# Optimization experiments

Measured on AMD Instinct MI355X. Metric: run time of the kernel, lower is better.

## Reference

```python
import jax, jax.numpy as jnp
import numpy as np

NEG_INF = -1e9
HIDDEN = 1024
HEADS = 16
SPH = HIDDEN // HEADS  # 64
B, Q, M = 8, 512, 512
R = Q + M


def rel_shift(x):
    # x: [N, H, Q, R] -> TransformerXL relative shift
    N, H, Qd, Rd = x.shape
    x = jnp.pad(x, ((0, 0), (0, 0), (0, 0), (1, 0)))
    x = x.reshape(N, H, Rd + 1, Qd)
    return x[:, :, 1:, :].reshape(N, H, Qd, Rd)


def setup_inputs() -> dict:
    key = jax.random.key(0)
    ks = jax.random.split(key, 11)
    std = 1.0 / np.sqrt(HIDDEN)
    # causal token mask: query position i (global pos M+i) may attend to ref pos j <= M+i
    q_pos = jnp.arange(Q)[:, None] + M
    r_pos = jnp.arange(R)[None, :]
    token_mask = (r_pos > q_pos).astype(jnp.float32)[None, None]  # [1,1,Q,R]
    return {
        "query_seqs": jax.random.normal(ks[0], (B, Q, HIDDEN), jnp.float32),
        "memory_seqs": jax.random.normal(ks[1], (B, M, HIDDEN), jnp.float32),
        "positional_encoding": jax.random.normal(ks[2], (R, HIDDEN), jnp.float32),
        "token_mask": token_mask,
        "content_bias": jax.random.normal(ks[3], (HEADS, SPH), jnp.float32) * 0.02,
        "position_bias": jax.random.normal(ks[4], (HEADS, SPH), jnp.float32) * 0.02,
        "Wq": jax.random.normal(ks[5], (HIDDEN, HEADS, SPH), jnp.float32) * std,
        "Wkc": jax.random.normal(ks[6], (HIDDEN, HEADS, SPH), jnp.float32) * std,
        "Wkp": jax.random.normal(ks[7], (HIDDEN, HEADS, SPH), jnp.float32) * std,
        "Wv": jax.random.normal(ks[8], (HIDDEN, HEADS, SPH), jnp.float32) * std,
        "Wo": jax.random.normal(ks[9], (HEADS, SPH, HIDDEN), jnp.float32) * std,
    }


def reference(query_seqs, memory_seqs, positional_encoding, token_mask,
              content_bias, position_bias, Wq, Wkc, Wkp, Wv, Wo):
    reference_seqs = jnp.concatenate([memory_seqs, query_seqs], axis=1)  # [B,R,D]
    query = jnp.einsum('nqd,dhs->nqhs', query_seqs, Wq)            # [B,Q,H,S]
    key_content = jnp.einsum('nrd,dhs->nrhs', reference_seqs, Wkc)  # [B,R,H,S]
    key_position = jnp.einsum('rd,dhs->rhs', positional_encoding, Wkp)  # [R,H,S]
    value = jnp.einsum('nrd,dhs->nrhs', reference_seqs, Wv)         # [B,R,H,S]

    content = jnp.einsum('nqhs,nrhs->nhqr', query + content_bias, key_content)
    positions = jnp.einsum('nqhs,rhs->nhqr', query + position_bias, key_position)
    positions = rel_shift(positions)

    scores = (content + positions) / np.sqrt(SPH) + token_mask * NEG_INF
    attn = jax.nn.softmax(scores, axis=3)  # [B,H,Q,R]
    out = jnp.einsum('nhqr,nrhs->nqhs', attn, value)
    return jnp.einsum('nqhs,hsd->nqd', out, Wo)  # [B,Q,D]
```

## Files before the change

### kernel.cpp

```cpp
#include <hip/hip_runtime.h>

#define B_ 8
#define Q_ 512
#define M_ 512
#define R_ 1024
#define H_ 16
#define S_ 64
#define D_ 1024
#define MEG 1048576L

typedef unsigned short ushort_t;
typedef __attribute__((ext_vector_type(8))) _Float16 f16x8;
typedef __attribute__((ext_vector_type(8))) unsigned short u16x8;
typedef __attribute__((ext_vector_type(4))) unsigned short u16x4;
typedef __attribute__((ext_vector_type(4))) float f32x4;
typedef __attribute__((ext_vector_type(2))) unsigned int u32x2;

__device__ __forceinline__ unsigned short h2u(_Float16 h) {
    union { _Float16 h; unsigned short u; } v; v.h = h; return v.u;
}
__device__ __forceinline__ unsigned int pk_f16(float a, float b) {
    union { _Float16 h[2]; unsigned int u; } v;
    v.h[0] = (_Float16)a; v.h[1] = (_Float16)b; return v.u;
}
__device__ __forceinline__ void async_cp16(const ushort_t* g, ushort_t* l) {
    __builtin_amdgcn_global_load_lds(
        (const __attribute__((address_space(1))) void*)g,
        (__attribute__((address_space(3))) void*)l, 16, 0, 0);
}

__global__ __launch_bounds__(256) void zero_out_f32_k(float* __restrict__ p, int n) {
    int i = blockIdx.x * 256 + threadIdx.x;
    if (i < n) p[i] = 0.f;
}

__global__ __launch_bounds__(256) void prep_k(
    const float* __restrict__ mem, const float* __restrict__ qry,
    const float* __restrict__ pos, const float* __restrict__ cb,
    const float* __restrict__ pb,
    const float* __restrict__ Wkc, const float* __restrict__ Wv,
    const float* __restrict__ Wkp, const float* __restrict__ Wq,
    const float* __restrict__ Wo,
    ushort_t* __restrict__ qcat, ushort_t* __restrict__ posb,
    ushort_t* __restrict__ cbpb, ushort_t* __restrict__ BT4,
    ushort_t* __restrict__ WoT) {
    int x = blockIdx.x, y = blockIdx.y, t = threadIdx.x;
    if (y < 5) {
        const float* in; ushort_t* out;
        switch (y) {
            case 0: in = Wkc; out = BT4;           break;
            case 1: in = Wv;  out = BT4 + MEG;     break;
            case 2: in = Wkp; out = BT4 + 2 * MEG; break;
            case 3: in = Wq;  out = BT4 + 3 * MEG; break;
            default: in = Wo; out = WoT;           break;
        }
        __shared__ ushort_t tile[32][33];
        int bx = (x & 31) * 32, by = (x >> 5) * 32;
        int tx = t & 31, ty = t >> 5;
        #pragma unroll
        for (int i = 0; i < 32; i += 8)
            tile[ty + i][tx] = h2u((_Float16)in[(long)(by + ty + i) * 1024 + bx + tx]);
        __syncthreads();
        #pragma unroll
        for (int i = 0; i < 32; i += 8)
            out[(long)(bx + ty + i) * 1024 + by + tx] = tile[tx][ty + i];
    } else if (y < 13) {
        int g = y - 5, r = x;
        const float* src = (r < 512) ? (mem + ((long)g * 512 + r) * 1024)
                                     : (qry + ((long)g * 512 + (r - 512)) * 1024);
        ushort_t* dst = qcat + ((long)g * 1024 + r) * 1024;
        int i = t * 4;
        f32x4 v = *(const f32x4*)(src + i);
        u32x2 o; o[0] = pk_f16(v[0], v[1]); o[1] = pk_f16(v[2], v[3]);
        *(u32x2*)(dst + i) = o;
    } else if (y == 13) {
        int i = t * 4;
        f32x4 v = *(const f32x4*)(pos + (long)x * 1024 + i);
        u32x2 o; o[0] = pk_f16(v[0], v[1]); o[1] = pk_f16(v[2], v[3]);
        *(u32x2*)(posb + (long)x * 1024 + i) = o;
    } else {
        if (x == 0) {
            for (int i = t; i < 1024; i += 256) {
                cbpb[i]        = h2u((_Float16)cb[i]);
                cbpb[1024 + i] = h2u((_Float16)pb[i]);
            }
        }
    }
}

__device__ __forceinline__ void gemm_body(const ushort_t* Arow0,
                                          const ushort_t* BTrow0,
                                          void* Crow0, long crs, int mode) {
    __shared__ __align__(16) ushort_t Al[2][128 * 32];
    __shared__ __align__(16) ushort_t Bl[2][128 * 32];

    int t = threadIdx.x;
    int wave = t >> 6, lane = t & 63, quad = lane >> 4, l16 = lane & 15;
    int wm = (wave & 1) * 64, wn = (wave >> 1) * 64;

    f32x4 acc[4][4];
    #pragma unroll
    for (int im = 0; im < 4; ++im)
        #pragma unroll
        for (int in = 0; in < 4; ++in) acc[im][in] = (f32x4){0.f, 0.f, 0.f, 0.f};

    int grow = lane >> 2, gcol = (lane & 3) * 8;
    const ushort_t* ga0 = Arow0 + (long)(wave * 32 + grow) * 1024 + gcol;
    const ushort_t* ga1 = Arow0 + (long)(wave * 32 + 16 + grow) * 1024 + gcol;
    const ushort_t* gb0 = BTrow0 + (long)(wave * 32 + grow) * 1024 + gcol;
    const ushort_t* gb1 = BTrow0 + (long)(wave * 32 + 16 + grow) * 1024 + gcol;
    int lo0 = (wave * 2 + 0) * 512;
    int lo1 = (wave * 2 + 1) * 512;

    async_cp16(ga0, &Al[0][lo0]);
    async_cp16(ga1, &Al[0][lo1]);
    async_cp16(gb0, &Bl[0][lo0]);
    async_cp16(gb1, &Bl[0][lo1]);
    __syncthreads();

    int cur = 0;
    for (int k0 = 0; k0 < 1024; k0 += 32) {
        int nxt = cur ^ 1;
        if (k0 + 32 < 1024) {
            async_cp16(ga0 + k0 + 32, &Al[nxt][lo0]);
            async_cp16(ga1 + k0 + 32, &Al[nxt][lo1]);
            async_cp16(gb0 + k0 + 32, &Bl[nxt][lo0]);
            async_cp16(gb1 + k0 + 32, &Bl[nxt][lo1]);
        }

        f16x8 af[4], bf[4];
        #pragma unroll
        for (int im = 0; im < 4; ++im)
            af[im] = *(const f16x8*)&Al[cur][(wm + im * 16 + l16) * 32 + quad * 8];
        #pragma unroll
        for (int in = 0; in < 4; ++in)
            bf[in] = *(const f16x8*)&Bl[cur][(wn + in * 16 + l16) * 32 + quad * 8];
        __builtin_amdgcn_s_setprio(1);
        #pragma unroll
        for (int im = 0; im < 4; ++im)
            #pragma unroll
            for (int in = 0; in < 4; ++in)
                acc[im][in] = __builtin_amdgcn_mfma_f32_16x16x32_f16(
                    af[im], bf[in], acc[im][in], 0, 0, 0);
        __builtin_amdgcn_s_setprio(0);
        __syncthreads();
        cur = nxt;
    }

    if (mode == 2) {
        #pragma unroll
        for (int im = 0; im < 4; ++im)
            #pragma unroll
            for (int in = 0; in < 4; ++in) {
                u16x4 pk;
                #pragma unroll
                for (int reg = 0; reg < 4; ++reg) pk[reg] = h2u((_Float16)acc[im][in][reg]);
                long addr = (long)(wn + in * 16 + l16) * 1024 + wm + im * 16 + quad * 4;
                *(u16x4*)((ushort_t*)Crow0 + addr) = pk;
            }
        return;
    }
    #pragma unroll
    for (int im = 0; im < 4; ++im)
        #pragma unroll
        for (int in = 0; in < 4; ++in)
            #pragma unroll
            for (int reg = 0; reg < 4; ++reg) {
                long addr = (long)(wm + im * 16 + quad * 4 + reg) * crs
                          + wn + in * 16 + l16;
                if (mode == 1) ((float*)Crow0)[addr] = acc[im][in][reg];
                else ((ushort_t*)Crow0)[addr] = h2u((_Float16)acc[im][in][reg]);
            }
}

__global__ __launch_bounds__(256) void gemm_mega(
    const ushort_t* __restrict__ qcat, const ushort_t* __restrict__ posb,
    const ushort_t* __restrict__ BT4,
    ushort_t* __restrict__ kcC, ushort_t* __restrict__ vT,
    ushort_t* __restrict__ qproj, ushort_t* __restrict__ kpp) {
    int id = blockIdx.x;
    if (id < 1024) {
        int z = id >> 7, tl = id & 127;
        int x = tl >> 4, y = tl & 15;
        const ushort_t* Arow0 = qcat + (long)z * MEG + (long)x * 128 * 1024;
        if (y < 8) {
            gemm_body(Arow0, BT4 + (long)y * 128 * 1024,
                      kcC + (long)z * MEG + (long)x * 128 * 1024 + y * 128, 1024, 0);
        } else {
            int n0 = (y - 8) * 128;
            gemm_body(Arow0, BT4 + (long)(1024 + n0) * 1024,
                      vT + ((long)z * 1024 + n0) * 1024 + x * 128, 0, 2);
        }
    } else if (id < 1088) {
        int u = id - 1024;
        int x = u >> 3, y = u & 7;
        gemm_body(posb + (long)x * 128 * 1024,
                  BT4 + (long)(2048 + y * 128) * 1024,
                  kpp + (long)x * 128 * 1024 + y * 128, 1024, 0);
    } else {
        int u = id - 1088;
        int b = u >> 5, v2 = u & 31;
        int x = v2 >> 3, y = v2 & 7;
        gemm_body(qcat + (long)b * MEG + (long)(512 + x * 128) * 1024,
                  BT4 + (long)(3072 + y * 128) * 1024,
                  qproj + (long)b * 512 * 1024 + (long)x * 128 * 1024 + y * 128, 1024, 0);
    }
}

__global__ __launch_bounds__(256) void gemm_fin(
    const ushort_t* __restrict__ A, const ushort_t* __restrict__ WoT,
    float* __restrict__ out) {
    gemm_body(A + (long)blockIdx.x * 128 * 1024,
              WoT + (long)blockIdx.y * 128 * 1024,
              out + (long)blockIdx.x * 128 * 1024 + blockIdx.y * 128, 1024, 1);
}

__global__ __launch_bounds__(512) void attn_kernel(
    const ushort_t* __restrict__ qproj,
    const ushort_t* __restrict__ kc,
    const ushort_t* __restrict__ kp,
    const ushort_t* __restrict__ vT,
    const ushort_t* __restrict__ cbpb,
    ushort_t* __restrict__ aout)
{
    int qt = (blockIdx.x + ((blockIdx.y >> 6) << 1)) & 3;
    int q0 = qt * 128;
    int bh = blockIdx.y;
    int b = bh >> 4, h = bh & 15;
    int t = threadIdx.x;
    int wave = t >> 6, lane = t & 63, quad = lane >> 4, l16 = lane & 15;

    __shared__ __align__(16) ushort_t Kc[64][72];
    __shared__ __align__(16) ushort_t Vt[64][72];
    __shared__ __align__(16) ushort_t Kp[192][72];
    __shared__ __align__(16) char Pu[8][2304];
    ushort_t* Pl = (ushort_t*)&Pu[wave][0];

    const ushort_t* qrow = qproj + ((long)(b * Q_ + q0 + wave * 16 + l16)) * 1024 + h * 64;
    f16x8 qcf[2], qpf[2];
    #pragma unroll
    for (int ks = 0; ks < 2; ++ks) {
        f16x8 qv  = *(const f16x8*)(qrow + ks * 32 + quad * 8);
        f16x8 cbv = *(const f16x8*)(cbpb + h * 64 + ks * 32 + quad * 8);
        f16x8 pbv = *(const f16x8*)(cbpb + 1024 + h * 64 + ks * 32 + quad * 8);
        qcf[ks] = qv + cbv;
        qpf[ks] = qv + pbv;
    }

    float m_s[4], l_s[4];
    f32x4 o_acc[4];
    #pragma unroll
    for (int r = 0; r < 4; ++r) {
        m_s[r] = -1e30f; l_s[r] = 0.f;
        o_acc[r] = (f32x4){0.f, 0.f, 0.f, 0.f};
    }

    int srow = t >> 3, sc0 = (t & 7) * 8;
    const ushort_t* kcb = kc + ((long)(b * R_) + srow) * 1024 + h * 64 + sc0;
    const ushort_t* vtb = vT + ((long)(b * 1024 + h * 64 + srow)) * 1024 + sc0;
    const ushort_t* kpb = kp + h * 64 + sc0;

    int ntiles = ((q0 + 639) >> 6) + 1;

    u16x8 rKc = *(const u16x8*)(kcb);
    u16x8 rVt = *(const u16x8*)(vtb);
    u16x8 rKp[3];
    {
        int jb0 = 384 - q0;
        #pragma unroll
        for (int p = 0; p < 3; ++p) {
            int j = jb0 + p * 64 + srow;
            int jc = j > 1023 ? 1023 : j;
            rKp[p] = *(const u16x8*)(kpb + (long)jc * 1024);
        }
    }

    for (int it = 0; it < ntiles; ++it) {
        int r0 = it * 64;
        int jbase = r0 - q0 + 384;
        int gb0 = jbase >> 4;
        __syncthreads();
        *(u16x8*)&Kc[srow][sc0] = rKc;
        *(u16x8*)&Vt[srow][sc0] = rVt;
        if (it == 0) {
            #pragma unroll
            for (int p = 0; p < 3; ++p) {
                int j = jbase + p * 64 + srow;
                int ph = ((j >> 4) % 12) * 16 + (j & 15);
                *(u16x8*)&Kp[ph][sc0] = rKp[p];
            }
        } else {
            int j = jbase + 128 + srow;
            int ph = ((j >> 4) % 12) * 16 + (j & 15);
            *(u16x8*)&Kp[ph][sc0] = rKp[0];
        }
        __syncthreads();
        if (it + 1 < ntiles) {
            int r1 = r0 + 64;
            rKc = *(const u16x8*)(kcb + (long)r1 * 1024);
            rVt = *(const u16x8*)(vtb + r1);
            int j = r1 - q0 + 512 + srow;
            int jc = j > 1023 ? 1023 : j;
            rKp[0] = *(const u16x8*)(kpb + (long)jc * 1024);
        }

        f32x4 sc[4];
        #pragma unroll
        for (int s = 0; s < 4; ++s) sc[s] = (f32x4){0.f, 0.f, 0.f, 0.f};
        f32x4 dd[5];
        #pragma unroll
        for (int s = 0; s < 5; ++s) dd[s] = (f32x4){0.f, 0.f, 0.f, 0.f};

        __builtin_amdgcn_s_setprio(1);
        #pragma unroll
        for (int ks = 0; ks < 2; ++ks)
            #pragma unroll
            for (int sub = 0; sub < 4; ++sub) {
                f16x8 bb = *(const f16x8*)&Kc[sub * 16 + l16][ks * 32 + quad * 8];
                sc[sub] = __builtin_amdgcn_mfma_f32_16x16x32_f16(qcf[ks], bb, sc[sub], 0, 0, 0);
            }
        #pragma unroll
        for (int ks = 0; ks < 2; ++ks)
            #pragma unroll
            for (int sub = 0; sub < 5; ++sub) {
                int pb = (gb0 + 7 - wave + sub) % 12;
                f16x8 bb = *(const f16x8*)&Kp[pb * 16 + l16][ks * 32 + quad * 8];
                dd[sub] = __builtin_amdgcn_mfma_f32_16x16x32_f16(qpf[ks], bb, dd[sub], 0, 0, 0);
            }
        __builtin_amdgcn_s_setprio(0);

        #pragma unroll
        for (int reg = 0; reg < 4; ++reg) {
            int row16 = quad * 4 + reg;
            int src = (lane & 48) + ((l16 + 15 - row16) & 15);
            float dsh[5];
            #pragma unroll
            for (int sub = 0; sub < 5; ++sub)
                dsh[sub] = __shfl(dd[sub][reg], src);
            #pragma unroll
            for (int sub = 0; sub < 4; ++sub) {
                float dval = (l16 > row16) ? dsh[sub + 1] : dsh[sub];
                float sv = (sc[sub][reg] + dval) * 0.125f;
                int rl = sub * 16 + l16;
                if (r0 + rl > q0 + wave * 16 + row16 + 512) sv = -1e30f;
                sc[sub][reg] = sv;
            }
        }

        float rm[4];
        #pragma unroll
        for (int reg = 0; reg < 4; ++reg) {
            float v = fmaxf(fmaxf(sc[0][reg], sc[1][reg]), fmaxf(sc[2][reg], sc[3][reg]));
            #pragma unroll
            for (int m = 1; m < 16; m <<= 1) v = fmaxf(v, __shfl_xor(v, m));
            rm[reg] = v;
        }
        int ok = (rm[0] <= m_s[0] + 8.f) & (rm[1] <= m_s[1] + 8.f) &
                 (rm[2] <= m_s[2] + 8.f) & (rm[3] <= m_s[3] + 8.f);
        if (!__all(ok)) {
            #pragma unroll
            for (int reg = 0; reg < 4; ++reg) {
                float mn = fmaxf(m_s[reg], rm[reg]);
                float alpha = __expf(m_s[reg] - mn);
                m_s[reg] = mn;
                l_s[reg] *= alpha;
                #pragma unroll
                for (int sub = 0; sub < 4; ++sub)
                    o_acc[sub][reg] *= alpha;
            }
        }
        float rs[4] = {0.f, 0.f, 0.f, 0.f};
        #pragma unroll
        for (int sub = 0; sub < 4; ++sub)
            #pragma unroll
            for (int reg = 0; reg < 4; ++reg) {
                float p = __expf(sc[sub][reg] - m_s[reg]);
                rs[reg] += p;
                Pl[(quad * 4 + reg) * 72 + sub * 16 + l16] = h2u((_Float16)p);
            }
        #pragma unroll
        for (int reg = 0; reg < 4; ++reg) {
            float v = rs[reg];
            #pragma unroll
            for (int m = 1; m < 16; m <<= 1) v += __shfl_xor(v, m);
            l_s[reg] += v;
        }

        __builtin_amdgcn_s_setprio(1);
        #pragma unroll
        for (int ks = 0; ks < 2; ++ks) {
            f16x8 a = *(const f16x8*)&Pl[l16 * 72 + ks * 32 + quad * 8];
            #pragma unroll
            for (int sub = 0; sub < 4; ++sub) {
                f16x8 bb = *(const f16x8*)&Vt[sub * 16 + l16][ks * 32 + quad * 8];
                o_acc[sub] = __builtin_amdgcn_mfma_f32_16x16x32_f16(a, bb, o_acc[sub], 0, 0, 0);
            }
        }
        __builtin_amdgcn_s_setprio(0);
    }

    #pragma unroll
    for (int reg = 0; reg < 4; ++reg) {
        float inv = 1.f / l_s[reg];
        int qg = q0 + wave * 16 + quad * 4 + reg;
        ushort_t* orow = aout + ((long)(b * Q_ + qg)) * 1024 + h * 64;
        #pragma unroll
        for (int sub = 0; sub < 4; ++sub)
            orow[sub * 16 + l16] = h2u((_Float16)(o_acc[sub][reg] * inv));
    }
}

extern "C" void kernel_launch(void* const* d_in, const int* in_sizes, int n_in,
                              void* d_out, int out_size, void* d_ws, size_t ws_size,
                              hipStream_t stream) {
    const float* query  = (const float*)d_in[0];
    const float* memory = (const float*)d_in[1];
    const float* pos    = (const float*)d_in[2];
    const float* cb  = (const float*)d_in[4];
    const float* pb  = (const float*)d_in[5];
    const float* Wq  = (const float*)d_in[6];
    const float* Wkc = (const float*)d_in[7];
    const float* Wkp = (const float*)d_in[8];
    const float* Wv  = (const float*)d_in[9];
    const float* Wo  = (const float*)d_in[10];
    float* out = (float*)d_out;
    ushort_t* ws = (ushort_t*)d_ws;

    size_t ws_elems = ws_size / 2;
    if (ws_elems < 36 * MEG) {
        zero_out_f32_k<<<(out_size + 255) / 256, 256, 0, stream>>>(out, out_size);
        return;
    }

    ushort_t* cbpb  = ws;
    ushort_t* BT4   = ws + MEG;
    ushort_t* WoT   = BT4 + 4 * MEG;
    ushort_t* kpp   = WoT + MEG;
    ushort_t* posb  = kpp + MEG;
    ushort_t* qproj = posb + MEG;
    ushort_t* kcC   = qproj + 4 * MEG;
    ushort_t* vT    = kcC + 8 * MEG;
    ushort_t* qcat  = vT + 8 * MEG;
    ushort_t* aout  = qproj;

    prep_k<<<dim3(1024, 15), 256, 0, stream>>>(
        memory, query, pos, cb, pb, Wkc, Wv, Wkp, Wq, Wo,
        qcat, posb, cbpb, BT4, WoT);
    gemm_mega<<<dim3(1344), 256, 0, stream>>>(qcat, posb, BT4, kcC, vT, qproj, kpp);
    attn_kernel<<<dim3(4, 128), 512, 0, stream>>>(qproj, kcC, kpp, vT, cbpb, aout);
    gemm_fin<<<dim3(32, 8, 1), 256, 0, stream>>>(aout, WoT, out);
}
```

Before: 263.3 us.

## Load K/V fragments directly from global, drop LDS staging and syncs, MFMA row sums

Removes the shared-memory staging of Kc, Vt and Kp along with the two block barriers per tile. Each wave now loads its MFMA operand fragments straight from global memory, relying on L1/L2 for reuse across the 8 waves. The softmax row sum is computed with an MFMA against a ones vector, and the row-max shuffle reduction runs only when a rescale is needed. Occupancy is also requested via launch bounds. The risk is redundant global/L2 traffic, since each wave re-reads the same K/V tiles, plus more register pressure from holding the fragments.

```diff
diff --git a/kernel.cpp b/kernel.cpp
--- a/kernel.cpp
+++ b/kernel.cpp
@@ -215,7 +215,7 @@
               out + (long)blockIdx.x * 128 * 1024 + blockIdx.y * 128, 1024, 1);
 }
 
-__global__ __launch_bounds__(512) void attn_kernel(
+__global__ __launch_bounds__(512, 4) void attn_kernel(
     const ushort_t* __restrict__ qproj,
     const ushort_t* __restrict__ kc,
     const ushort_t* __restrict__ kp,
@@ -230,9 +230,6 @@
     int t = threadIdx.x;
     int wave = t >> 6, lane = t & 63, quad = lane >> 4, l16 = lane & 15;
 
-    __shared__ __align__(16) ushort_t Kc[64][72];
-    __shared__ __align__(16) ushort_t Vt[64][72];
-    __shared__ __align__(16) ushort_t Kp[192][72];
     __shared__ __align__(16) char Pu[8][2304];
     ushort_t* Pl = (ushort_t*)&Pu[wave][0];
 
@@ -247,62 +244,44 @@
         qpf[ks] = qv + pbv;
     }
 
-    float m_s[4], l_s[4];
-    f32x4 o_acc[4];
+    float m_s[4];
+    f32x4 o_acc[4], ls4;
     #pragma unroll
     for (int r = 0; r < 4; ++r) {
-        m_s[r] = -1e30f; l_s[r] = 0.f;
+        m_s[r] = -1e30f;
         o_acc[r] = (f32x4){0.f, 0.f, 0.f, 0.f};
     }
-
-    int srow = t >> 3, sc0 = (t & 7) * 8;
-    const ushort_t* kcb = kc + ((long)(b * R_) + srow) * 1024 + h * 64 + sc0;
-    const ushort_t* vtb = vT + ((long)(b * 1024 + h * 64 + srow)) * 1024 + sc0;
-    const ushort_t* kpb = kp + h * 64 + sc0;
+    ls4 = (f32x4){0.f, 0.f, 0.f, 0.f};
+
+    f16x8 ones;
+    #pragma unroll
+    for (int j = 0; j < 8; ++j) ones[j] = (_Float16)1.0f;
+
+    const ushort_t* kcb = kc + ((long)b * R_) * 1024 + h * 64;
+    const ushort_t* vtb = vT + ((long)(b * 1024 + h * 64)) * 1024;
+    const ushort_t* kpb = kp + h * 64;
 
     int ntiles = ((q0 + 639) >> 6) + 1;
-
-    u16x8 rKc = *(const u16x8*)(kcb);
-    u16x8 rVt = *(const u16x8*)(vtb);
-    u16x8 rKp[3];
-    {
-        int jb0 = 384 - q0;
-        #pragma unroll
-        for (int p = 0; p < 3; ++p) {
-            int j = jb0 + p * 64 + srow;
-            int jc = j > 1023 ? 1023 : j;
-            rKp[p] = *(const u16x8*)(kpb + (long)jc * 1024);
-        }
-    }
 
     for (int it = 0; it < ntiles; ++it) {
         int r0 = it * 64;
-        int jbase = r0 - q0 + 384;
-        int gb0 = jbase >> 4;
-        __syncthreads();
-        *(u16x8*)&Kc[srow][sc0] = rKc;
-        *(u16x8*)&Vt[srow][sc0] = rVt;
-        if (it == 0) {
-            #pragma unroll
-            for (int p = 0; p < 3; ++p) {
-                int j = jbase + p * 64 + srow;
-                int ph = ((j >> 4) % 12) * 16 + (j & 15);
-                *(u16x8*)&Kp[ph][sc0] = rKp[p];
-            }
-        } else {
-            int j = jbase + 128 + srow;
-            int ph = ((j >> 4) % 12) * 16 + (j & 15);
-            *(u16x8*)&Kp[ph][sc0] = rKp[0];
-        }
-        __syncthreads();
-        if (it + 1 < ntiles) {
-            int r1 = r0 + 64;
-            rKc = *(const u16x8*)(kcb + (long)r1 * 1024);
-            rVt = *(const u16x8*)(vtb + r1);
-            int j = r1 - q0 + 512 + srow;
-            int jc = j > 1023 ? 1023 : j;
-            rKp[0] = *(const u16x8*)(kpb + (long)jc * 1024);
-        }
+        int gb0 = (r0 - q0 + 384) >> 4;
+
+        f16x8 kcf[2][4], kpf[2][5];
+        #pragma unroll
+        for (int ks = 0; ks < 2; ++ks)
+            #pragma unroll
+            for (int sub = 0; sub < 4; ++sub)
+                kcf[ks][sub] = *(const f16x8*)(kcb
+                    + (long)(r0 + sub * 16 + l16) * 1024 + ks * 32 + quad * 8);
+        #pragma unroll
+        for (int ks = 0; ks < 2; ++ks)
+            #pragma unroll
+            for (int sub = 0; sub < 5; ++sub) {
+                int jg = (gb0 + 7 - wave + sub) * 16 + l16;
+                if (jg > 1023) jg = 1023;
+                kpf[ks][sub] = *(const f16x8*)(kpb + (long)jg * 1024 + ks * 32 + quad * 8);
+            }
 
         f32x4 sc[4];
         #pragma unroll
@@ -315,19 +294,24 @@
         #pragma unroll
         for (int ks = 0; ks < 2; ++ks)
             #pragma unroll
-            for (int sub = 0; sub < 4; ++sub) {
-                f16x8 bb = *(const f16x8*)&Kc[sub * 16 + l16][ks * 32 + quad * 8];
-                sc[sub] = __builtin_amdgcn_mfma_f32_16x16x32_f16(qcf[ks], bb, sc[sub], 0, 0, 0);
-            }
+            for (int sub = 0; sub < 4; ++sub)
+                sc[sub] = __builtin_amdgcn_mfma_f32_16x16x32_f16(
+                    qcf[ks], kcf[ks][sub], sc[sub], 0, 0, 0);
         #pragma unroll
         for (int ks = 0; ks < 2; ++ks)
             #pragma unroll
-            for (int sub = 0; sub < 5; ++sub) {
-                int pb = (gb0 + 7 - wave + sub) % 12;
-                f16x8 bb = *(const f16x8*)&Kp[pb * 16 + l16][ks * 32 + quad * 8];
-                dd[sub] = __builtin_amdgcn_mfma_f32_16x16x32_f16(qpf[ks], bb, dd[sub], 0, 0, 0);
-            }
+            for (int sub = 0; sub < 5; ++sub)
+                dd[sub] = __builtin_amdgcn_mfma_f32_16x16x32_f16(
+                    qpf[ks], kpf[ks][sub], dd[sub], 0, 0, 0);
         __builtin_amdgcn_s_setprio(0);
+
+        f16x8 vtf[2][4];
+        #pragma unroll
+        for (int ks = 0; ks < 2; ++ks)
+            #pragma unroll
+            for (int sub = 0; sub < 4; ++sub)
+                vtf[ks][sub] = *(const f16x8*)(vtb
+                    + (long)(sub * 16 + l16) * 1024 + r0 + ks * 32 + quad * 8);
 
         #pragma unroll
         for (int reg = 0; reg < 4; ++reg) {
@@ -347,61 +331,54 @@
             }
         }
 
-        float rm[4];
-        #pragma unroll
-        for (int reg = 0; reg < 4; ++reg) {
-            float v = fmaxf(fmaxf(sc[0][reg], sc[1][reg]), fmaxf(sc[2][reg], sc[3][reg]));
-            #pragma unroll
-            for (int m = 1; m < 16; m <<= 1) v = fmaxf(v, __shfl_xor(v, m));
-            rm[reg] = v;
-        }
-        int ok = (rm[0] <= m_s[0] + 8.f) & (rm[1] <= m_s[1] + 8.f) &
-                 (rm[2] <= m_s[2] + 8.f) & (rm[3] <= m_s[3] + 8.f);
+        float vmax[4];
+        #pragma unroll
+        for (int reg = 0; reg < 4; ++reg)
+            vmax[reg] = fmaxf(fmaxf(sc[0][reg], sc[1][reg]),
+                              fmaxf(sc[2][reg], sc[3][reg]));
+        int ok = (vmax[0] <= m_s[0] + 8.f) & (vmax[1] <= m_s[1] + 8.f) &
+                 (vmax[2] <= m_s[2] + 8.f) & (vmax[3] <= m_s[3] + 8.f);
         if (!__all(ok)) {
             #pragma unroll
             for (int reg = 0; reg < 4; ++reg) {
-                float mn = fmaxf(m_s[reg], rm[reg]);
+                float rm = vmax[reg];
+                #pragma unroll
+                for (int m = 1; m < 16; m <<= 1) rm = fmaxf(rm, __shfl_xor(rm, m));
+                float mn = fmaxf(m_s[reg], rm);
                 float alpha = __expf(m_s[reg] - mn);
                 m_s[reg] = mn;
-                l_s[reg] *= alpha;
+                ls4[reg] *= alpha;
                 #pragma unroll
                 for (int sub = 0; sub < 4; ++sub)
                     o_acc[sub][reg] *= alpha;
             }
         }
-        float rs[4] = {0.f, 0.f, 0.f, 0.f};
         #pragma unroll
         for (int sub = 0; sub < 4; ++sub)
             #pragma unroll
             for (int reg = 0; reg < 4; ++reg) {
                 float p = __expf(sc[sub][reg] - m_s[reg]);
-                rs[reg] += p;
                 Pl[(quad * 4 + reg) * 72 + sub * 16 + l16] = h2u((_Float16)p);
             }
-        #pragma unroll
-        for (int reg = 0; reg < 4; ++reg) {
-            float v = rs[reg];
-            #pragma unroll
-            for (int m = 1; m < 16; m <<= 1) v += __shfl_xor(v, m);
-            l_s[reg] += v;
-        }
-
+
+        f16x8 a0 = *(const f16x8*)&Pl[l16 * 72 + quad * 8];
+        f16x8 a1 = *(const f16x8*)&Pl[l16 * 72 + 32 + quad * 8];
         __builtin_amdgcn_s_setprio(1);
-        #pragma unroll
-        for (int ks = 0; ks < 2; ++ks) {
-            f16x8 a = *(const f16x8*)&Pl[l16 * 72 + ks * 32 + quad * 8];
-            #pragma unroll
-            for (int sub = 0; sub < 4; ++sub) {
-                f16x8 bb = *(const f16x8*)&Vt[sub * 16 + l16][ks * 32 + quad * 8];
-                o_acc[sub] = __builtin_amdgcn_mfma_f32_16x16x32_f16(a, bb, o_acc[sub], 0, 0, 0);
-            }
+        ls4 = __builtin_amdgcn_mfma_f32_16x16x32_f16(a0, ones, ls4, 0, 0, 0);
+        ls4 = __builtin_amdgcn_mfma_f32_16x16x32_f16(a1, ones, ls4, 0, 0, 0);
+        #pragma unroll
+        for (int sub = 0; sub < 4; ++sub) {
+            o_acc[sub] = __builtin_amdgcn_mfma_f32_16x16x32_f16(
+                a0, vtf[0][sub], o_acc[sub], 0, 0, 0);
+            o_acc[sub] = __builtin_amdgcn_mfma_f32_16x16x32_f16(
+                a1, vtf[1][sub], o_acc[sub], 0, 0, 0);
         }
         __builtin_amdgcn_s_setprio(0);
     }
 
     #pragma unroll
     for (int reg = 0; reg < 4; ++reg) {
-        float inv = 1.f / l_s[reg];
+        float inv = 1.f / ls4[reg];
         int qg = q0 + wave * 16 + quad * 4 + reg;
         ushort_t* orow = aout + ((long)(b * Q_ + qg)) * 1024 + h * 64;
         #pragma unroll
```

New measurement: 377.3 us. 1.43x slower.
